# Performance work log

Measured on AMD Instinct MI355X. Metric: run time of the kernel, lower is better.

## Reference

```python
import jax, jax.numpy as jnp
import numpy as np

N, M, A, O, F = 4, 64, 64, 5, 256


def _sph_harm_l2(R):
    # real spherical harmonics up to l=2 (9 components) of the unit direction
    r = jnp.linalg.norm(R, axis=-1, keepdims=True)
    u = R / (r + 1e-12)
    x, y, z = u[..., 0], u[..., 1], u[..., 2]
    c1 = 0.4886025119029199
    c2 = 1.0925484305920792
    return jnp.stack([
        jnp.full_like(x, 0.28209479177387814),
        c1 * y, c1 * z, c1 * x,
        c2 * x * y, c2 * y * z,
        0.31539156525252005 * (3.0 * z * z - 1.0),
        c2 * x * z,
        0.5462742152960396 * (x * x - y * y),
    ], axis=-1)  # [..., 9]


def setup_inputs() -> dict:
    key = jax.random.key(0)
    ks = jax.random.split(key, 6)
    return {
        "ao_embeddings": jax.random.normal(ks[0], (N, M, A, O, F), jnp.float32),
        "C": jax.random.normal(ks[1], (N, M, A, O), jnp.float32),
        "S": jax.random.normal(ks[2], (N, A, 3, A, 3), jnp.float32),
        "R": jax.random.normal(ks[3], (N, M, A, 3), jnp.float32),
        "w_stack": jax.random.normal(ks[4], (5, 3, 3), jnp.float32) * 0.5,
        "cgc": jax.random.normal(ks[5], (9, 9, 9), jnp.float32) * 0.1,
    }


def reference(ao_embeddings, C, S, R, w_stack, cgc):
    # mo_features: [n, m, a, o=5, f]
    mo = C[..., None] * ao_embeddings
    # 5-step bilinear transform of the overlap-like tensor S [n, a, 3, b, 3]
    Sc = S
    for i in range(5):
        w = w_stack[i]  # [3, 3]
        Sc = jnp.einsum('ab,cd,kibjd->kiajc', w, w, Sc)
        Sc = jax.nn.swish(Sc)
    filt = jnp.array([[1., 1., 0.], [1., 1., 0.], [0., 0., 1.]], Sc.dtype)
    Sc = filt[None, None, :, None, :] * Sc
    idx = jnp.array([0, 1, 2, 2, 2])  # tf.repeat(repeats=[1, 1, 3]) -> size 5
    Sc = jnp.take(jnp.take(Sc, idx, axis=2), idx, axis=4)  # [n, a, 5, b, 5]
    # message passing over atom pairs: [n, m, b, p=5, f]
    mo = jnp.einsum('nmaof,naobp->nmbpf', mo, Sc)
    # unsorted_segment_sum with segment_ids [0,0,1,2,3] into 9 slots == matmul with one-hot map
    seg = jnp.zeros((5, 9), mo.dtype).at[jnp.arange(5), jnp.array([0, 0, 1, 2, 3])].set(1.0)
    mo = jnp.einsum('nmbpf,pq->nmbqf', mo, seg)  # [n, m, a, 9, f]
    # coupling: sph harmonics * ||C|| (tf.repeat over f == broadcast, folded into einsum)
    Cn = jnp.linalg.norm(C, axis=-1)            # [n, m, a]
    coup = _sph_harm_l2(R) * Cn[..., None]      # [n, m, a, 9]
    # CG contraction + sum over atoms a: [n, m, i=9, f]
    out = jnp.einsum('nmapf,nmak,kip->nmif', mo, coup, cgc)
    return jnp.transpose(out, (0, 1, 3, 2))     # [n, m, f, 9]
```

## Files before the change

### kernel.cpp

```cpp
#include <hip/hip_runtime.h>
#include <math.h>


typedef float v4f __attribute__((ext_vector_type(4)));
static __device__ inline v4f splat4(float s) { return (v4f){s, s, s, s}; }

__global__ void k_sc(const float* __restrict__ S, const float* __restrict__ wst,
                     float* __restrict__ G) {
    int t = blockIdx.x * 128 + threadIdx.x;
    int n = t >> 12;
    int a = (t >> 6) & 63;
    int b = t & 63;
    float M[3][3];
#pragma unroll
    for (int x = 0; x < 3; ++x)
#pragma unroll
        for (int y = 0; y < 3; ++y)
            M[x][y] = S[(((n * 64 + a) * 3 + x) * 64 + b) * 3 + y];
#pragma unroll
    for (int it = 0; it < 5; ++it) {
        float w[3][3];
#pragma unroll
        for (int x = 0; x < 3; ++x)
#pragma unroll
            for (int y = 0; y < 3; ++y)
                w[x][y] = wst[it * 9 + x * 3 + y];
        float T[3][3];
#pragma unroll
        for (int x = 0; x < 3; ++x)
#pragma unroll
            for (int d = 0; d < 3; ++d)
                T[x][d] = w[x][0] * M[0][d] + w[x][1] * M[1][d] + w[x][2] * M[2][d];
#pragma unroll
        for (int x = 0; x < 3; ++x)
#pragma unroll
            for (int c = 0; c < 3; ++c) {
                float v = T[x][0] * w[c][0] + T[x][1] * w[c][1] + T[x][2] * w[c][2];
                M[x][c] = v / (1.f + expf(-v));
            }
    }
    float g0 = M[0][0] + M[0][1];
    float g1 = M[1][0] + M[1][1];
    float gz = M[2][2];
    size_t base = (size_t)n * 12288 + (size_t)b * 64 + a;
    G[base]          = g0;
    G[base + 4096]   = g1;
    G[base + 8192]   = gz;
}

__global__ __launch_bounds__(512, 4) void k_go(
        const float* __restrict__ ao, const float* __restrict__ C,
        const float* __restrict__ R, const float* __restrict__ cgc,
        const float* __restrict__ G, float* __restrict__ out) {
    __shared__ float s_coup[64 * 9];
    __shared__ float s_D[2 * 9 * 64];
    __shared__ float s_W3[64 * 28];
    __shared__ float s_C[320];

    const int bid = blockIdx.x;
    const int nm = bid >> 1;
    const int fh = bid & 1;
    const int n = nm >> 6;
    const int tid = threadIdx.x;
    const int w = tid >> 6;
    const int lane = tid & 63;
    const int fgrp = lane & 3;
    const int agrp = lane >> 2;
    const int f0 = fh * 128 + w * 16 + fgrp * 4;
    const float* ap = ao + (size_t)nm * 81920 + (size_t)agrp * 1280 + f0;

    v4f cur[5];
#pragma unroll
    for (int o = 0; o < 5; ++o)
        cur[o] = *(const v4f*)(ap + o * 256);

    for (int e = tid; e < 320; e += 512) s_C[e] = C[(size_t)nm * 320 + e];
    if (tid < 64) {
        const int b = tid;
        const float* rp = R + ((size_t)nm * 64 + b) * 3;
        float x = rp[0], y = rp[1], z = rp[2];
        float rn = sqrtf(x * x + y * y + z * z) + 1e-12f;
        x /= rn; y /= rn; z /= rn;
        const float* cp = C + ((size_t)nm * 64 + b) * 5;
        float cn = 0.f;
#pragma unroll
        for (int o = 0; o < 5; ++o) cn += cp[o] * cp[o];
        cn = sqrtf(cn);
        const float c1 = 0.4886025119029199f;
        const float c2 = 1.0925484305920792f;
        float Y[9];
        Y[0] = 0.28209479177387814f;
        Y[1] = c1 * y;
        Y[2] = c1 * z;
        Y[3] = c1 * x;
        Y[4] = c2 * x * y;
        Y[5] = c2 * y * z;
        Y[6] = 0.31539156525252005f * (3.f * z * z - 1.f);
        Y[7] = c2 * x * z;
        Y[8] = 0.5462742152960396f * (x * x - y * y);
#pragma unroll
        for (int k = 0; k < 9; ++k) s_coup[b * 9 + k] = Y[k] * cn;
    }
    __syncthreads();

    for (int e = tid; e < 576; e += 512) {
        const int b = e & 63, i = e >> 6;
        float d0 = 0.f, dz = 0.f;
#pragma unroll
        for (int k = 0; k < 9; ++k) {
            float cp = s_coup[b * 9 + k];
            const float* cg = cgc + k * 81 + i * 9;
            d0 = fmaf(cp, cg[0], d0);
            dz = fmaf(cp, cg[1] + cg[2] + cg[3], dz);
        }
        s_D[(0 * 9 + i) * 64 + b] = d0;
        s_D[(1 * 9 + i) * 64 + b] = dz;
    }
    __syncthreads();

    for (int pp = w; pp < 9; pp += 8) {
        const int u = pp / 3;
        const int i0 = (pp % 3) * 3;
        const int pm = (u == 2) ? 1 : 0;
        const float* gp = G + (size_t)n * 12288 + (size_t)u * 4096 + lane;
        const float* dp = &s_D[(pm * 9 + i0) * 64];
        float a0 = 0.f, a1 = 0.f, a2 = 0.f;
#pragma unroll 8
        for (int b = 0; b < 64; ++b) {
            float g = gp[b * 64];
            a0 = fmaf(g, dp[b], a0);
            a1 = fmaf(g, dp[64 + b], a1);
            a2 = fmaf(g, dp[128 + b], a2);
        }
        s_W3[lane * 28 + u * 9 + i0 + 0] = a0;
        s_W3[lane * 28 + u * 9 + i0 + 1] = a1;
        s_W3[lane * 28 + u * 9 + i0 + 2] = a2;
    }
    __syncthreads();

    v4f acc[9];
#pragma unroll
    for (int i = 0; i < 9; ++i) acc[i] = splat4(0.f);

#pragma unroll
    for (int t = 0; t < 4; ++t) {
        v4f nxt[5];
        if (t < 3) {
            const float* apn = ap + (t + 1) * 20480;
#pragma unroll
            for (int o = 0; o < 5; ++o)
                nxt[o] = *(const v4f*)(apn + o * 256);
        }
        const int a = agrp + 16 * t;
        const float* cc = &s_C[a * 5];
        v4f e0 = splat4(cc[0]) * cur[0];
        v4f e1 = splat4(cc[1]) * cur[1];
        v4f e2 = splat4(cc[2]) * cur[2] + splat4(cc[3]) * cur[3] + splat4(cc[4]) * cur[4];
        const float* w3 = &s_W3[a * 28];
#pragma unroll
        for (int i = 0; i < 9; ++i)
            acc[i] += splat4(w3[i]) * e0 + splat4(w3[9 + i]) * e1 + splat4(w3[18 + i]) * e2;
        if (t < 3) {
#pragma unroll
            for (int o = 0; o < 5; ++o) cur[o] = nxt[o];
        }
    }

#pragma unroll
    for (int mask = 4; mask <= 32; mask <<= 1) {
#pragma unroll
        for (int i = 0; i < 9; ++i) {
#pragma unroll
            for (int j = 0; j < 4; ++j)
                acc[i][j] += __shfl_xor(acc[i][j], mask, 64);
        }
    }

    if (agrp == 0) {
        v4f buf4[9];
        float* bp = (float*)buf4;
#pragma unroll
        for (int j = 0; j < 4; ++j)
#pragma unroll
            for (int i = 0; i < 9; ++i)
                bp[j * 9 + i] = acc[i][j];
        float* op = out + (size_t)nm * 2304 + (size_t)f0 * 9;
#pragma unroll
        for (int q = 0; q < 9; ++q)
            *(v4f*)(op + q * 4) = buf4[q];
    }
}

extern "C" void kernel_launch(void* const* d_in, const int* in_sizes, int n_in,
                              void* d_out, int out_size, void* d_ws, size_t ws_size,
                              hipStream_t stream) {
    (void)in_sizes; (void)n_in; (void)out_size; (void)ws_size;
    const float* ao  = (const float*)d_in[0];
    const float* C   = (const float*)d_in[1];
    const float* S   = (const float*)d_in[2];
    const float* R   = (const float*)d_in[3];
    const float* wst = (const float*)d_in[4];
    const float* cgc = (const float*)d_in[5];
    float* out = (float*)d_out;
    float* G = (float*)d_ws;

    hipLaunchKernelGGL(k_sc, dim3(128), dim3(128), 0, stream, S, wst, G);
    hipLaunchKernelGGL(k_go, dim3(512), dim3(512), 0, stream,
                       ao, C, R, cgc, G, out);
}
```

Before: 31.52 us.

## Restructure main kernel: one block per (n,m), precombined C*W3 rows, LDS cross-wave reduction

Each block now covers all 256 features of one (n,m) instead of half. Each wave takes 40 of the 320 (a,o) rows, and each lane handles 4 features. A premultiplied table K = C*W3 per (a,o) row is built in LDS, so the inner loop is 9 vector FMAs per row instead of recombining 5 orbitals. Partial sums are reduced across the 8 waves through a large LDS buffer rather than shuffles. The cost is more LDS use (about 95KB) and half as many blocks, which lowers occupancy. The duplicated preamble work per (n,m) is removed.

```diff
diff --git a/kernel.cpp b/kernel.cpp
--- a/kernel.cpp
+++ b/kernel.cpp
@@ -48,31 +48,28 @@
     G[base + 8192]   = gz;
 }
 
-__global__ __launch_bounds__(512, 4) void k_go(
+__global__ __launch_bounds__(512) void k_go(
         const float* __restrict__ ao, const float* __restrict__ C,
         const float* __restrict__ R, const float* __restrict__ cgc,
         const float* __restrict__ G, float* __restrict__ out) {
-    __shared__ float s_coup[64 * 9];
-    __shared__ float s_D[2 * 9 * 64];
+    __shared__ float s_coup[576];
+    __shared__ float s_D[1152];
     __shared__ float s_W3[64 * 28];
     __shared__ float s_C[320];
-
-    const int bid = blockIdx.x;
-    const int nm = bid >> 1;
-    const int fh = bid & 1;
+    __shared__ float s_K[320 * 12];
+    __shared__ float s_par[8 * 2368];
+
+    const int nm = blockIdx.x;
     const int n = nm >> 6;
     const int tid = threadIdx.x;
     const int w = tid >> 6;
     const int lane = tid & 63;
-    const int fgrp = lane & 3;
-    const int agrp = lane >> 2;
-    const int f0 = fh * 128 + w * 16 + fgrp * 4;
-    const float* ap = ao + (size_t)nm * 81920 + (size_t)agrp * 1280 + f0;
-
-    v4f cur[5];
-#pragma unroll
-    for (int o = 0; o < 5; ++o)
-        cur[o] = *(const v4f*)(ap + o * 256);
+
+    const float* aw = ao + (size_t)nm * 81920 + (size_t)(w * 40) * 256 + lane * 4;
+    v4f b0 = *(const v4f*)(aw + 0 * 256);
+    v4f b1 = *(const v4f*)(aw + 1 * 256);
+    v4f b2 = *(const v4f*)(aw + 2 * 256);
+    v4f b3 = *(const v4f*)(aw + 3 * 256);
 
     for (int e = tid; e < 320; e += 512) s_C[e] = C[(size_t)nm * 320 + e];
     if (tid < 64) {
@@ -138,56 +135,61 @@
     }
     __syncthreads();
 
+    for (int e = tid; e < 2880; e += 512) {
+        int r = e / 9, i = e - r * 9;
+        int a = r / 5, o = r - a * 5;
+        int u = o < 2 ? o : 2;
+        s_K[r * 12 + i] = s_C[r] * s_W3[a * 28 + u * 9 + i];
+    }
+    __syncthreads();
+
     v4f acc[9];
 #pragma unroll
     for (int i = 0; i < 9; ++i) acc[i] = splat4(0.f);
-
-#pragma unroll
-    for (int t = 0; t < 4; ++t) {
-        v4f nxt[5];
-        if (t < 3) {
-            const float* apn = ap + (t + 1) * 20480;
-#pragma unroll
-            for (int o = 0; o < 5; ++o)
-                nxt[o] = *(const v4f*)(apn + o * 256);
-        }
-        const int a = agrp + 16 * t;
-        const float* cc = &s_C[a * 5];
-        v4f e0 = splat4(cc[0]) * cur[0];
-        v4f e1 = splat4(cc[1]) * cur[1];
-        v4f e2 = splat4(cc[2]) * cur[2] + splat4(cc[3]) * cur[3] + splat4(cc[4]) * cur[4];
-        const float* w3 = &s_W3[a * 28];
-#pragma unroll
-        for (int i = 0; i < 9; ++i)
-            acc[i] += splat4(w3[i]) * e0 + splat4(w3[9 + i]) * e1 + splat4(w3[18 + i]) * e2;
-        if (t < 3) {
-#pragma unroll
-            for (int o = 0; o < 5; ++o) cur[o] = nxt[o];
-        }
-    }
-
-#pragma unroll
-    for (int mask = 4; mask <= 32; mask <<= 1) {
-#pragma unroll
-        for (int i = 0; i < 9; ++i) {
-#pragma unroll
-            for (int j = 0; j < 4; ++j)
-                acc[i][j] += __shfl_xor(acc[i][j], mask, 64);
-        }
-    }
-
-    if (agrp == 0) {
-        v4f buf4[9];
-        float* bp = (float*)buf4;
+    const int rbase = w * 40;
+
+#define ROW_STEP(BUF, T_OFF)                                              \
+    {                                                                     \
+        const float* Kp = &s_K[(rbase + 4 * tt + (T_OFF)) * 12];          \
+        v4f k0 = *(const v4f*)(Kp);                                       \
+        v4f k1 = *(const v4f*)(Kp + 4);                                   \
+        float k8 = Kp[8];                                                 \
+        acc[0] += splat4(k0.x) * BUF;                                     \
+        acc[1] += splat4(k0.y) * BUF;                                     \
+        acc[2] += splat4(k0.z) * BUF;                                     \
+        acc[3] += splat4(k0.w) * BUF;                                     \
+        acc[4] += splat4(k1.x) * BUF;                                     \
+        acc[5] += splat4(k1.y) * BUF;                                     \
+        acc[6] += splat4(k1.z) * BUF;                                     \
+        acc[7] += splat4(k1.w) * BUF;                                     \
+        acc[8] += splat4(k8) * BUF;                                       \
+        if (tt < 9) BUF = *(const v4f*)(aw + (4 * tt + (T_OFF) + 4) * 256); \
+    }
+
+    for (int tt = 0; tt < 10; ++tt) {
+        ROW_STEP(b0, 0)
+        ROW_STEP(b1, 1)
+        ROW_STEP(b2, 2)
+        ROW_STEP(b3, 3)
+    }
+#undef ROW_STEP
+
+    {
+        float* sp = &s_par[w * 2368 + lane * 37];
 #pragma unroll
         for (int j = 0; j < 4; ++j)
 #pragma unroll
             for (int i = 0; i < 9; ++i)
-                bp[j * 9 + i] = acc[i][j];
-        float* op = out + (size_t)nm * 2304 + (size_t)f0 * 9;
-#pragma unroll
-        for (int q = 0; q < 9; ++q)
-            *(v4f*)(op + q * 4) = buf4[q];
+                sp[j * 9 + i] = acc[i][j];
+    }
+    __syncthreads();
+    for (int s = tid; s < 2304; s += 512) {
+        int f = s / 9, i = s - f * 9;
+        int off = (f >> 2) * 37 + (f & 3) * 9 + i;
+        float sum = 0.f;
+#pragma unroll
+        for (int w2 = 0; w2 < 8; ++w2) sum += s_par[w2 * 2368 + off];
+        out[(size_t)nm * 2304 + s] = sum;
     }
 }
 
@@ -205,6 +207,6 @@
     float* G = (float*)d_ws;
 
     hipLaunchKernelGGL(k_sc, dim3(128), dim3(128), 0, stream, S, wst, G);
-    hipLaunchKernelGGL(k_go, dim3(512), dim3(512), 0, stream,
+    hipLaunchKernelGGL(k_go, dim3(256), dim3(512), 0, stream,
                        ao, C, R, cgc, G, out);
 }
```

New measurement: 29.17 us. 7.5% less time.
